# Optimization experiments

Measured on AMD Instinct MI355X. Metric: run time of the kernel, lower is better.

The kernel has to match this reference:

```python
import jax, jax.numpy as jnp
import numpy as np

DIM = 128
N_NODES = 100000
N_EDGES = 640000


def setup_inputs() -> dict:
    key = jax.random.key(0)
    k1, k2, k3, k4, k5, k6 = jax.random.split(key, 6)
    x = jax.random.normal(k1, (N_NODES, DIM), dtype=jnp.float32)
    edge_index = jax.random.randint(k2, (2, N_EDGES), 0, N_NODES, dtype=jnp.int64)
    edge_weight = jax.random.uniform(k3, (N_EDGES,), dtype=jnp.float32)
    # Linear(dim, dim) params (PyTorch stores weight as [out, in])
    bound = 1.0 / np.sqrt(DIM)
    W = jax.random.uniform(k4, (DIM, DIM), minval=-bound, maxval=bound, dtype=jnp.float32)
    b = jax.random.uniform(k5, (DIM,), minval=-bound, maxval=bound, dtype=jnp.float32)
    alpha = jnp.float32(0.5)
    return {"x": x, "edge_index": edge_index, "num_nodes": N_NODES,
            "edge_weight": edge_weight, "W": W, "b": b, "alpha": alpha}


def reference(x, edge_index, num_nodes, edge_weight, W, b, alpha):
    src = edge_index[0]
    dst = edge_index[1]
    msg = x[src] * edge_weight[:, None]                      # [E, D] gather + weight
    agg = jax.ops.segment_sum(msg, dst, num_segments=num_nodes)   # [N, D] scatter-add
    deg = jax.ops.segment_sum(jnp.ones_like(edge_weight), dst, num_segments=num_nodes)
    deg = jnp.maximum(deg, 1.0)                              # clamp(min=1.0)
    agg = agg / deg[:, None]                                 # mean normalization
    return x + alpha * (agg @ W.T + b)                       # linear + alpha residual
```

## Files before the change

### kernel.cpp

```cpp
#include <hip/hip_runtime.h>
#include <hip/hip_bf16.h>

#define DIM 128
#define NPB 512
#define NPB_SHIFT 9

#define A1_EPT 8
#define A1_EPB (256 * A1_EPT)
#define NBLK_STRIDE 512

#define FROWS 64
#define FPAD 136

typedef __attribute__((ext_vector_type(8))) short bf16x8;
typedef __attribute__((ext_vector_type(8))) unsigned short u16x8;
typedef __attribute__((ext_vector_type(4))) float f32x4;

__device__ __forceinline__ short f2bf(float f) {
    union { __hip_bfloat16 h; short s; } u;
    u.h = __float2bfloat16(f);
    return u.s;
}
__device__ __forceinline__ float bf2f(unsigned short s) {
    union { unsigned int u; float f; } c;
    c.u = ((unsigned int)s) << 16;
    return c.f;
}

__device__ __forceinline__ int load_dst(const void* eidx, int flag64, int E, int e) {
    return flag64 ? (int)((const long long*)eidx)[E + e] : ((const int*)eidx)[E + e];
}
__device__ __forceinline__ int load_src(const void* eidx, int flag64, int E, int e) {
    return flag64 ? (int)((const long long*)eidx)[e] : ((const int*)eidx)[e];
}

__device__ __forceinline__ int detect64_block(const unsigned int* e, int* sdet) {
    if (threadIdx.x == 0) {
        int ok64 = 1;
        for (int t = 0; t < 128; ++t) {
            if (e[2 * t + 1] != 0u) { ok64 = 0; break; }
        }
        *sdet = ok64;
    }
    __syncthreads();
    return *sdet;
}

__global__ __launch_bounds__(256) void prep_kernel(
        const float* __restrict__ x, unsigned short* __restrict__ xb, int n8,
        const void* __restrict__ eidx, int* __restrict__ bhistT, int E, int nblk) {
    __shared__ int bcnt[256];
    __shared__ int sdet;
    const int tid = threadIdx.x;
    const int blk = blockIdx.x;
    const bool hist = (blk < nblk);

    int f = 0;
    if (hist) {
        f = detect64_block((const unsigned int*)eidx, &sdet);
        bcnt[tid] = 0;
        __syncthreads();
        const int base = blk * A1_EPB;
        #pragma unroll
        for (int i = 0; i < A1_EPT; ++i) {
            int e = base + tid + i * 256;
            if (e < E) atomicAdd(&bcnt[load_dst(eidx, f, E, e) >> NPB_SHIFT], 1);
        }
    }

    const int stride = gridDim.x * blockDim.x;
    for (int t = blk * blockDim.x + tid; t < n8; t += stride) {
        const float4* pp = (const float4*)(x + (size_t)t * 8);
        float4 a = pp[0], b = pp[1];
        u16x8 o;
        o[0] = (unsigned short)f2bf(a.x); o[1] = (unsigned short)f2bf(a.y);
        o[2] = (unsigned short)f2bf(a.z); o[3] = (unsigned short)f2bf(a.w);
        o[4] = (unsigned short)f2bf(b.x); o[5] = (unsigned short)f2bf(b.y);
        o[6] = (unsigned short)f2bf(b.z); o[7] = (unsigned short)f2bf(b.w);
        *(u16x8*)(xb + (size_t)t * 8) = o;
    }

    if (hist) {
        __syncthreads();
        bhistT[tid * NBLK_STRIDE + blk] = bcnt[tid];
    }
}

__global__ __launch_bounds__(512) void scancol_kernel(
        int* __restrict__ bhistT, int* __restrict__ colsum, int nblk) {
    __shared__ int s[512];
    const int tid = threadIdx.x;
    const int bu = blockIdx.x;
    int v = (tid < nblk) ? bhistT[bu * NBLK_STRIDE + tid] : 0;
    s[tid] = v;
    __syncthreads();
    for (int off = 1; off < 512; off <<= 1) {
        int t = (tid >= off) ? s[tid - off] : 0;
        __syncthreads();
        s[tid] += t;
        __syncthreads();
    }
    if (tid < nblk) bhistT[bu * NBLK_STRIDE + tid] = s[tid] - v;
    if (tid == 511) colsum[bu] = s[511];
}

__global__ __launch_bounds__(256) void scanb_kernel(
        const int* __restrict__ colsum, int* __restrict__ gstart, int NB, int E) {
    __shared__ int s[256];
    const int tid = threadIdx.x;
    int val = (tid < NB) ? colsum[tid] : 0;
    s[tid] = val;
    __syncthreads();
    for (int off = 1; off < 256; off <<= 1) {
        int t = (tid >= off) ? s[tid - off] : 0;
        __syncthreads();
        s[tid] += t;
        __syncthreads();
    }
    if (tid < NB) gstart[tid] = s[tid] - val;
    if (tid == NB) gstart[NB] = E;
}

__global__ __launch_bounds__(256) void part2_kernel(
        const void* __restrict__ eidx, const float* __restrict__ ew,
        const int* __restrict__ bhistT, const int* __restrict__ gstart,
        unsigned long long* __restrict__ srcw_tmp, int E) {
    __shared__ unsigned long long stage[A1_EPB];
    __shared__ unsigned char sbid[A1_EPB];
    __shared__ int bcnt[256], bscan[256], bcur[256], brun[256];
    __shared__ int sdet;
    const int tid = threadIdx.x;
    const int blk = blockIdx.x;
    const int base = blk * A1_EPB;
    const int f = detect64_block((const unsigned int*)eidx, &sdet);

    bcnt[tid] = 0;
    __syncthreads();

    unsigned long long pk[A1_EPT];
    unsigned char bid[A1_EPT];
    #pragma unroll
    for (int i = 0; i < A1_EPT; ++i) {
        int e = base + tid + i * 256;
        bid[i] = 0xFF;
        if (e < E) {
            int src = load_src(eidx, f, E, e);
            int dst = load_dst(eidx, f, E, e);
            unsigned int w = __float_as_uint(ew[e]);
            int b = dst >> NPB_SHIFT;
            pk[i] = ((unsigned long long)w << 26)
                  | ((unsigned long long)(dst & (NPB - 1)) << 17)
                  | (unsigned long long)(unsigned)src;
            bid[i] = (unsigned char)b;
            atomicAdd(&bcnt[b], 1);
        }
    }
    __syncthreads();

    int val = bcnt[tid];
    bscan[tid] = val;
    __syncthreads();
    for (int off = 1; off < 256; off <<= 1) {
        int t = (tid >= off) ? bscan[tid - off] : 0;
        __syncthreads();
        bscan[tid] += t;
        __syncthreads();
    }
    int excl = bscan[tid] - val;
    __syncthreads();
    bscan[tid] = excl;
    bcur[tid] = excl;
    brun[tid] = gstart[tid] + bhistT[tid * NBLK_STRIDE + blk];
    __syncthreads();

    #pragma unroll
    for (int i = 0; i < A1_EPT; ++i) {
        if (bid[i] != 0xFF) {
            int slot = atomicAdd(&bcur[bid[i]], 1);
            stage[slot] = pk[i];
            sbid[slot] = bid[i];
        }
    }
    __syncthreads();

    int tot = (base + A1_EPB <= E) ? A1_EPB : (E - base);
    for (int s = tid; s < tot; s += 256) {
        int b = sbid[s];
        srcw_tmp[brun[b] + (s - bscan[b])] = stage[s];
    }
}

__global__ __launch_bounds__(512) void sort_kernel(
        const unsigned long long* __restrict__ srcw_tmp,
        const int* __restrict__ gstart, unsigned long long* __restrict__ srcw,
        int* __restrict__ rowstart, int nn) {
    __shared__ int cnt[NPB], cur[NPB], s[NPB];
    const int tid = threadIdx.x;
    const int b = blockIdx.x;
    const int node0 = b << NPB_SHIFT;
    const int e0 = gstart[b], e1 = gstart[b + 1];

    cnt[tid] = 0;
    __syncthreads();
    for (int e = e0 + tid; e < e1; e += 512)
        atomicAdd(&cnt[(int)((srcw_tmp[e] >> 17) & (NPB - 1))], 1);
    __syncthreads();

    int val = cnt[tid];
    s[tid] = val;
    __syncthreads();
    for (int off = 1; off < 512; off <<= 1) {
        int t = (tid >= off) ? s[tid - off] : 0;
        __syncthreads();
        s[tid] += t;
        __syncthreads();
    }
    int excl = s[tid] - val;
    cur[tid] = excl;
    __syncthreads();

    int nbn = nn - node0; if (nbn > NPB) nbn = NPB;
    if (tid < nbn) rowstart[node0 + tid] = e0 + excl;

    for (int e = e0 + tid; e < e1; e += 512) {
        unsigned long long pk = srcw_tmp[e];
        int dl = (int)((pk >> 17) & (NPB - 1));
        int pos = e0 + atomicAdd(&cur[dl], 1);
        srcw[pos] = ((pk >> 26) << 32) | (pk & 0x1FFFFULL);
    }
}

__global__ __launch_bounds__(256) void gather_kernel(
        const unsigned short* __restrict__ xb, const uint2* __restrict__ srcw,
        const int* __restrict__ rowstart, unsigned short* __restrict__ aggb,
        int nn, int E) {
    int g = (blockIdx.x * blockDim.x + threadIdx.x) >> 4;
    int sub16 = threadIdx.x & 15;
    if (g >= nn) return;
    int n0 = rowstart[g];
    int n1 = (g + 1 < nn) ? rowstart[g + 1] : E;
    float acc[8] = {0.f, 0.f, 0.f, 0.f, 0.f, 0.f, 0.f, 0.f};
    for (int e = n0; e < n1; e += 8) {
        int rem = n1 - e;
        uint2 sws[8];
        #pragma unroll
        for (int i = 0; i < 8; ++i) {
            if (i < rem) sws[i] = srcw[e + i];
            else { sws[i].x = 0u; sws[i].y = 0u; }
        }
        u16x8 xs[8];
        #pragma unroll
        for (int i = 0; i < 8; ++i)
            xs[i] = *(const u16x8*)(xb + (size_t)sws[i].x * DIM + sub16 * 8);
        #pragma unroll
        for (int i = 0; i < 8; ++i) {
            float w = __uint_as_float(sws[i].y);
            #pragma unroll
            for (int j = 0; j < 8; ++j)
                acc[j] = fmaf(bf2f(xs[i][j]), w, acc[j]);
        }
    }
    float inv = 1.0f / fmaxf((float)(n1 - n0), 1.0f);
    u16x8 o;
    #pragma unroll
    for (int j = 0; j < 8; ++j) o[j] = (unsigned short)f2bf(acc[j] * inv);
    *(u16x8*)(aggb + (size_t)g * DIM + sub16 * 8) = o;
}

__global__ __launch_bounds__(512) void finish_kernel(
        const unsigned short* __restrict__ aggb, float* __restrict__ out,
        const unsigned short* __restrict__ xb, const float* __restrict__ W,
        const float* __restrict__ bias, const float* __restrict__ alphaP, int nn) {
    __shared__ alignas(16) unsigned short A_lds[FROWS * FPAD];
    const int tid  = threadIdx.x;
    const int wv   = tid >> 6;
    const int lane = tid & 63;
    const int half = lane >> 4;
    const int l16  = lane & 15;
    const int b0   = blockIdx.x * FROWS;
    const float alpha = alphaP[0];

    const int jcol = wv * 16 + l16;
    bf16x8 bfrag[4];
    #pragma unroll
    for (int kt = 0; kt < 4; ++kt) {
        const float4* w4 = (const float4*)(W + (size_t)jcol * DIM + kt * 32 + half * 8);
        float4 lo = w4[0], hi = w4[1];
        bf16x8 b;
        b[0] = f2bf(lo.x); b[1] = f2bf(lo.y); b[2] = f2bf(lo.z); b[3] = f2bf(lo.w);
        b[4] = f2bf(hi.x); b[5] = f2bf(hi.y); b[6] = f2bf(hi.z); b[7] = f2bf(hi.w);
        bfrag[kt] = b;
    }
    const float bias_j = bias[jcol];

    #pragma unroll
    for (int it = 0; it < 2; ++it) {
        int p = it * 512 + tid;
        int row = p >> 4;
        int c8 = p & 15;
        int node = b0 + row;
        u16x8 v = {0, 0, 0, 0, 0, 0, 0, 0};
        if (node < nn) v = *(const u16x8*)(aggb + (size_t)node * DIM + c8 * 8);
        *(u16x8*)&A_lds[row * FPAD + c8 * 8] = v;
    }
    __syncthreads();

    #pragma unroll
    for (int mt = 0; mt < 4; ++mt) {
        f32x4 acc = {0.f, 0.f, 0.f, 0.f};
        #pragma unroll
        for (int kt = 0; kt < 4; ++kt) {
            const bf16x8 a = *(const bf16x8*)&A_lds[(mt * 16 + l16) * FPAD + kt * 32 + half * 8];
            acc = __builtin_amdgcn_mfma_f32_16x16x32_bf16(a, bfrag[kt], acc, 0, 0, 0);
        }
        #pragma unroll
        for (int r = 0; r < 4; ++r) {
            int grow = b0 + mt * 16 + half * 4 + r;
            if (grow < nn) {
                size_t idx = (size_t)grow * DIM + jcol;
                out[idx] = bf2f(xb[idx]) + alpha * (acc[r] + bias_j);
            }
        }
    }
}

extern "C" void kernel_launch(void* const* d_in, const int* in_sizes, int n_in,
                              void* d_out, int out_size, void* d_ws, size_t ws_size,
                              hipStream_t stream) {
    const float* x      = (const float*)d_in[0];
    const void*  eidx   = d_in[1];
    const float* ew     = (const float*)d_in[3];
    const float* W      = (const float*)d_in[4];
    const float* bias   = (const float*)d_in[5];
    const float* alphaP = (const float*)d_in[6];

    const int NN = in_sizes[0] / DIM;
    const int E  = in_sizes[3];
    const int NB = (NN + NPB - 1) / NPB;
    const int nblk = (E + A1_EPB - 1) / A1_EPB;

    unsigned short* aggb = (unsigned short*)d_ws;
    unsigned short* xb   = aggb + (size_t)NN * DIM;
    unsigned long long* srcw     = (unsigned long long*)(xb + (size_t)NN * DIM);
    unsigned long long* srcw_tmp = srcw + E;
    int* rowstart = (int*)(srcw_tmp + E);
    int* bhistT   = rowstart + NN;
    int* colsum   = bhistT + 256 * NBLK_STRIDE;
    int* gstart   = colsum + 256;

    float* out = (float*)d_out;

    int n8 = NN * DIM / 8;
    prep_kernel<<<2048, 256, 0, stream>>>(x, xb, n8, eidx, bhistT, E, nblk);

    scancol_kernel<<<NB, 512, 0, stream>>>(bhistT, colsum, nblk);

    scanb_kernel<<<1, 256, 0, stream>>>(colsum, gstart, NB, E);

    part2_kernel<<<nblk, 256, 0, stream>>>(eidx, ew, bhistT, gstart, srcw_tmp, E);

    sort_kernel<<<NB, 512, 0, stream>>>(srcw_tmp, gstart, srcw, rowstart, NN);

    int gblocks = (NN + 15) / 16;
    gather_kernel<<<gblocks, 256, 0, stream>>>(xb, (const uint2*)srcw, rowstart,
                                               aggb, NN, E);

    int fblocks = (NN + FROWS - 1) / FROWS;
    finish_kernel<<<fblocks, 512, 0, stream>>>(aggb, out, xb, W, bias, alphaP, NN);
}
```

Before: 101.9 us.

## Fuse neighbor gather aggregation into the MFMA linear finish kernel

Merges the gather kernel into the finish kernel. Each block now aggregates its 64 nodes' neighbor rows directly into LDS (8 threads per node, 16 columns each) before the bf16 MFMA linear step. This drops the bf16 agg round trip through global memory and one kernel launch. In exchange, gather parallelism per block changes, with fewer lanes per row and 4-edge batches, and MFMA work now waits on the slowest node's gather within each block.

```diff
diff --git a/kernel.cpp b/kernel.cpp
--- a/kernel.cpp
+++ b/kernel.cpp
@@ -230,54 +230,68 @@
     }
 }
 
-__global__ __launch_bounds__(256) void gather_kernel(
+__global__ __launch_bounds__(512) void gf_kernel(
         const unsigned short* __restrict__ xb, const uint2* __restrict__ srcw,
-        const int* __restrict__ rowstart, unsigned short* __restrict__ aggb,
-        int nn, int E) {
-    int g = (blockIdx.x * blockDim.x + threadIdx.x) >> 4;
-    int sub16 = threadIdx.x & 15;
-    if (g >= nn) return;
-    int n0 = rowstart[g];
-    int n1 = (g + 1 < nn) ? rowstart[g + 1] : E;
-    float acc[8] = {0.f, 0.f, 0.f, 0.f, 0.f, 0.f, 0.f, 0.f};
-    for (int e = n0; e < n1; e += 8) {
-        int rem = n1 - e;
-        uint2 sws[8];
-        #pragma unroll
-        for (int i = 0; i < 8; ++i) {
-            if (i < rem) sws[i] = srcw[e + i];
-            else { sws[i].x = 0u; sws[i].y = 0u; }
-        }
-        u16x8 xs[8];
-        #pragma unroll
-        for (int i = 0; i < 8; ++i)
-            xs[i] = *(const u16x8*)(xb + (size_t)sws[i].x * DIM + sub16 * 8);
-        #pragma unroll
-        for (int i = 0; i < 8; ++i) {
-            float w = __uint_as_float(sws[i].y);
-            #pragma unroll
-            for (int j = 0; j < 8; ++j)
-                acc[j] = fmaf(bf2f(xs[i][j]), w, acc[j]);
-        }
-    }
-    float inv = 1.0f / fmaxf((float)(n1 - n0), 1.0f);
-    u16x8 o;
-    #pragma unroll
-    for (int j = 0; j < 8; ++j) o[j] = (unsigned short)f2bf(acc[j] * inv);
-    *(u16x8*)(aggb + (size_t)g * DIM + sub16 * 8) = o;
-}
-
-__global__ __launch_bounds__(512) void finish_kernel(
-        const unsigned short* __restrict__ aggb, float* __restrict__ out,
-        const unsigned short* __restrict__ xb, const float* __restrict__ W,
-        const float* __restrict__ bias, const float* __restrict__ alphaP, int nn) {
+        const int* __restrict__ rowstart, float* __restrict__ out,
+        const float* __restrict__ W, const float* __restrict__ bias,
+        const float* __restrict__ alphaP, int nn, int E) {
     __shared__ alignas(16) unsigned short A_lds[FROWS * FPAD];
-    const int tid  = threadIdx.x;
+    const int tid = threadIdx.x;
+    const int b0  = blockIdx.x * FROWS;
+
+    {
+        const int r  = tid >> 3;
+        const int ls = tid & 7;
+        const int g  = b0 + r;
+        float acc[16];
+        #pragma unroll
+        for (int j = 0; j < 16; ++j) acc[j] = 0.f;
+        float inv = 1.0f;
+        if (g < nn) {
+            int n0 = rowstart[g];
+            int n1 = (g + 1 < nn) ? rowstart[g + 1] : E;
+            for (int e = n0; e < n1; e += 4) {
+                int rem = n1 - e;
+                uint2 sws[4];
+                #pragma unroll
+                for (int i = 0; i < 4; ++i) {
+                    if (i < rem) sws[i] = srcw[e + i];
+                    else { sws[i].x = 0u; sws[i].y = 0u; }
+                }
+                u16x8 lo[4], hi[4];
+                #pragma unroll
+                for (int i = 0; i < 4; ++i) {
+                    const u16x8* xp = (const u16x8*)(xb + (size_t)sws[i].x * DIM + ls * 16);
+                    lo[i] = xp[0];
+                    hi[i] = xp[1];
+                }
+                #pragma unroll
+                for (int i = 0; i < 4; ++i) {
+                    float w = __uint_as_float(sws[i].y);
+                    #pragma unroll
+                    for (int j = 0; j < 8; ++j) {
+                        acc[j]     = fmaf(bf2f(lo[i][j]), w, acc[j]);
+                        acc[j + 8] = fmaf(bf2f(hi[i][j]), w, acc[j + 8]);
+                    }
+                }
+            }
+            inv = 1.0f / fmaxf((float)(n1 - n0), 1.0f);
+        }
+        u16x8 o0, o1;
+        #pragma unroll
+        for (int j = 0; j < 8; ++j) {
+            o0[j] = (unsigned short)f2bf(acc[j] * inv);
+            o1[j] = (unsigned short)f2bf(acc[j + 8] * inv);
+        }
+        *(u16x8*)&A_lds[r * FPAD + ls * 16] = o0;
+        *(u16x8*)&A_lds[r * FPAD + ls * 16 + 8] = o1;
+    }
+    __syncthreads();
+
     const int wv   = tid >> 6;
     const int lane = tid & 63;
     const int half = lane >> 4;
     const int l16  = lane & 15;
-    const int b0   = blockIdx.x * FROWS;
     const float alpha = alphaP[0];
 
     const int jcol = wv * 16 + l16;
@@ -294,18 +308,6 @@
     const float bias_j = bias[jcol];
 
     #pragma unroll
-    for (int it = 0; it < 2; ++it) {
-        int p = it * 512 + tid;
-        int row = p >> 4;
-        int c8 = p & 15;
-        int node = b0 + row;
-        u16x8 v = {0, 0, 0, 0, 0, 0, 0, 0};
-        if (node < nn) v = *(const u16x8*)(aggb + (size_t)node * DIM + c8 * 8);
-        *(u16x8*)&A_lds[row * FPAD + c8 * 8] = v;
-    }
-    __syncthreads();
-
-    #pragma unroll
     for (int mt = 0; mt < 4; ++mt) {
         f32x4 acc = {0.f, 0.f, 0.f, 0.f};
         #pragma unroll
@@ -339,8 +341,7 @@
     const int NB = (NN + NPB - 1) / NPB;
     const int nblk = (E + A1_EPB - 1) / A1_EPB;
 
-    unsigned short* aggb = (unsigned short*)d_ws;
-    unsigned short* xb   = aggb + (size_t)NN * DIM;
+    unsigned short* xb = (unsigned short*)d_ws;
     unsigned long long* srcw     = (unsigned long long*)(xb + (size_t)NN * DIM);
     unsigned long long* srcw_tmp = srcw + E;
     int* rowstart = (int*)(srcw_tmp + E);
@@ -361,10 +362,7 @@
 
     sort_kernel<<<NB, 512, 0, stream>>>(srcw_tmp, gstart, srcw, rowstart, NN);
 
-    int gblocks = (NN + 15) / 16;
-    gather_kernel<<<gblocks, 256, 0, stream>>>(xb, (const uint2*)srcw, rowstart,
-                                               aggb, NN, E);
-
     int fblocks = (NN + FROWS - 1) / FROWS;
-    finish_kernel<<<fblocks, 512, 0, stream>>>(aggb, out, xb, W, bias, alphaP, NN);
-}
+    gf_kernel<<<fblocks, 512, 0, stream>>>(xb, (const uint2*)srcw, rowstart,
+                                           out, W, bias, alphaP, NN, E);
+}
```

Result: no change. 102.5 us (+0.6%).
